# Performance work log

Measured on AMD Instinct MI355X. Metric: run time of the kernel, lower is better.

The kernel has to match this reference:

```python
import jax, jax.numpy as jnp
import numpy as np

B, N, DIM, H, DH = 2, 2048, 512, 8, 64
INNER = H * DH


def setup_inputs() -> dict:
    key = jax.random.key(0)
    ks = jax.random.split(key, 6)
    x = jax.random.normal(ks[0], (B, N, DIM), dtype=jnp.float32)
    mask_np = jax.random.randint(ks[1], (B, N), 0, 2, dtype=jnp.int32)
    mask_bert = jax.random.randint(ks[2], (B, N), 0, 2, dtype=jnp.int32)
    # params (torch Linear(dim, 3*inner, bias=False) -> stored here as [in, out])
    s_in = 1.0 / np.sqrt(DIM)
    s_inner = 1.0 / np.sqrt(INNER)
    W_qkv = jax.random.uniform(ks[3], (DIM, 3 * INNER), jnp.float32, -s_in, s_in)
    W_out = jax.random.uniform(ks[4], (INNER, DIM), jnp.float32, -s_inner, s_inner)
    b_out = jax.random.uniform(ks[5], (DIM,), jnp.float32, -s_inner, s_inner)
    return {"x": x, "mask_np": mask_np, "mask_bert": mask_bert,
            "W_qkv": W_qkv, "W_out": W_out, "b_out": b_out}


def reference(x, mask_np, mask_bert, W_qkv, W_out, b_out):
    scale = DH ** -0.5
    qkv = x @ W_qkv                                   # [b, n, 3*inner]
    q, k, v = jnp.split(qkv, 3, axis=-1)
    split_heads = lambda t: t.reshape(B, N, H, DH).transpose(0, 2, 1, 3)  # b h n d
    q, k, v = split_heads(q), split_heads(k), split_heads(v)
    dots = jnp.einsum('bhid,bhjd->bhij', q, k) * scale  # [b, h, n, n]
    # dual mask: (np_i * np_j == 0) or (bert_j == 1) -> fill with -1000
    np_pair = mask_np[:, None, :, None] * mask_np[:, None, None, :]      # b 1 n n
    bert_j = mask_bert[:, None, None, :]                                  # b 1 1 n
    masked = (np_pair == 0) | (bert_j == 1)
    dots = jnp.where(masked, jnp.float32(-1000.0), dots)
    attn = jax.nn.softmax(dots, axis=-1)
    out = jnp.einsum('bhij,bhjd->bhid', attn, v)       # b h n d
    out = out.transpose(0, 2, 1, 3).reshape(B, N, INNER)
    return out @ W_out + b_out
```

## Files before the change

kernel.cpp:

```cpp
#include <hip/hip_runtime.h>

typedef __attribute__((ext_vector_type(8))) short short8;
typedef __attribute__((ext_vector_type(4))) float f32x4;

#define GLDS16(gp, lp)                                                                     \
  __builtin_amdgcn_global_load_lds(                                                        \
      (const __attribute__((address_space(1))) unsigned int*)(gp),                         \
      (__attribute__((address_space(3))) unsigned int*)(lp), 16, 0, 0)

__device__ __forceinline__ unsigned short f2bf(float f) {
  unsigned u = __float_as_uint(f);
  u += 0x7FFFu + ((u >> 16) & 1u);
  return (unsigned short)(u >> 16);
}
__device__ __forceinline__ float bf2f(unsigned short h) {
  return __uint_as_float(((unsigned)h) << 16);
}
__device__ __forceinline__ unsigned cvt_pk_bf16(float a, float b) {
  unsigned r;
  asm("v_cvt_pk_bf16_f32 %0, %1, %2" : "=v"(r) : "v"(a), "v"(b));
  return r;
}

#define QSCALE 0.1803368801111244f

__global__ __launch_bounds__(256) void prep_x(
    const float* __restrict__ x, const int* __restrict__ mnp, const int* __restrict__ mbert,
    unsigned short* __restrict__ xb, unsigned short* __restrict__ jmbf) {
  int tid = blockIdx.x * 256 + threadIdx.x;
  if (tid < 524288) {
    float4 v = *(const float4*)(x + tid * 4);
    ushort4 o;
    o.x = f2bf(v.x); o.y = f2bf(v.y); o.z = f2bf(v.z); o.w = f2bf(v.w);
    *(ushort4*)(xb + tid * 4) = o;
  } else {
    int o = tid - 524288;
    if (o < 4096) jmbf[o] = (mnp[o] == 0 || mbert[o] == 1) ? f2bf(-100.0f) : f2bf(1e30f);
  }
}

__global__ __launch_bounds__(256) void transpose_w(
    const float* __restrict__ wqkv, const float* __restrict__ wout,
    unsigned short* __restrict__ wqkvT, unsigned short* __restrict__ whiT,
    unsigned short* __restrict__ wloT) {
  __shared__ float tile[64][65];
  int bid = blockIdx.x;
  const float* src;
  int N, k0, n0, which;
  if (bid < 192) { which = 0; src = wqkv; N = 1536; k0 = (bid / 24) * 64; n0 = (bid % 24) * 64; }
  else { bid -= 192; which = 1; src = wout; N = 512; k0 = (bid / 8) * 64; n0 = (bid % 8) * 64; }
  int tx = threadIdx.x & 63, ty = threadIdx.x >> 6;
#pragma unroll
  for (int i = 0; i < 16; ++i) {
    int row = ty + i * 4;
    tile[row][tx] = src[(k0 + row) * N + n0 + tx];
  }
  __syncthreads();
#pragma unroll
  for (int i = 0; i < 16; ++i) {
    int row = ty + i * 4;
    float w = tile[tx][row];
    if (which == 0) {
      wqkvT[(n0 + row) * 512 + k0 + tx] = f2bf(w);
    } else {
      unsigned short hi = f2bf(w);
      whiT[(n0 + row) * 512 + k0 + tx] = hi;
      wloT[(n0 + row) * 512 + k0 + tx] = f2bf(w - bf2f(hi));
    }
  }
}

__global__ __launch_bounds__(256) void qkv_gemm(
    const unsigned short* __restrict__ A, const unsigned short* __restrict__ Bt,
    unsigned short* __restrict__ qb, unsigned short* __restrict__ kb,
    unsigned short* __restrict__ vtb) {
  __shared__ __attribute__((aligned(16))) unsigned short lA[2][64 * 64];
  __shared__ __attribute__((aligned(16))) unsigned short lB[2][128 * 64];
  const int lane = threadIdx.x & 63, wid = threadIdx.x >> 6;
  const int l15 = lane & 15, lg = lane >> 4;
  const int row0 = blockIdx.x * 64;
  const int col0 = blockIdx.y * 128;
  const int srow = lane >> 3;
  const int gslot = (lane & 7) ^ srow;
  f32x4 acc[4][2] = {};

#define QKV_STAGE(ks_, buf_)                                                               \
  {                                                                                        \
    const int k0_ = (ks_) * 64;                                                            \
    _Pragma("unroll") for (int i = 0; i < 2; ++i) {                                        \
      int c = wid * 2 + i;                                                                 \
      GLDS16(A + (row0 + c * 8 + srow) * 512 + k0_ + gslot * 8, &lA[buf_][c * 512]);       \
    }                                                                                      \
    _Pragma("unroll") for (int i = 0; i < 4; ++i) {                                        \
      int c = wid * 4 + i;                                                                 \
      GLDS16(Bt + (col0 + c * 8 + srow) * 512 + k0_ + gslot * 8, &lB[buf_][c * 512]);      \
    }                                                                                      \
  }

  QKV_STAGE(0, 0);
  int buf = 0;
  for (int ks = 0; ks < 8; ++ks) {
    if (ks < 7) {
      QKV_STAGE(ks + 1, buf ^ 1);
      asm volatile("s_waitcnt vmcnt(6)" ::: "memory");
    } else {
      asm volatile("s_waitcnt vmcnt(0)" ::: "memory");
    }
    __builtin_amdgcn_s_barrier();
    const unsigned short* La = &lA[buf][0];
    const unsigned short* Lb = &lB[buf][0];
#pragma unroll
    for (int ksub = 0; ksub < 2; ++ksub) {
      short8 af[4], bfr[2];
#pragma unroll
      for (int m = 0; m < 4; ++m) {
        int row = m * 16 + l15;
        int slot = (ksub * 4 + lg) ^ (row & 7);
        af[m] = *(const short8*)(La + row * 64 + slot * 8);
      }
#pragma unroll
      for (int n = 0; n < 2; ++n) {
        int row = wid * 32 + n * 16 + l15;
        int slot = (ksub * 4 + lg) ^ (row & 7);
        bfr[n] = *(const short8*)(Lb + row * 64 + slot * 8);
      }
#pragma unroll
      for (int m = 0; m < 4; ++m)
#pragma unroll
        for (int n = 0; n < 2; ++n)
          acc[m][n] = __builtin_amdgcn_mfma_f32_16x16x32_bf16(af[m], bfr[n], acc[m][n], 0, 0, 0);
    }
    __builtin_amdgcn_s_barrier();
    buf ^= 1;
  }

  if (col0 >= 1024) {
    unsigned short* T = &lB[0][0];
#pragma unroll
    for (int m = 0; m < 4; ++m)
#pragma unroll
      for (int n = 0; n < 2; ++n) {
        int lc = wid * 32 + n * 16 + l15;
#pragma unroll
        for (int r = 0; r < 4; ++r)
          T[lc * 72 + m * 16 + lg * 4 + r] = f2bf(acc[m][n][r]);
      }
    __syncthreads();
    int c = threadIdx.x >> 1, half = threadIdx.x & 1;
    int gcol = col0 + c;
    int hh = (gcol >> 6) & 7, d = gcol & 63;
    int b = row0 >> 11, np0 = row0 & 2047;
    unsigned short* dst = vtb + ((size_t)((b * 8 + hh) * 64 + d)) * 2048 + np0 + half * 32;
    const unsigned short* srcT = T + c * 72 + half * 32;
#pragma unroll
    for (int i = 0; i < 4; ++i)
      *(short8*)(dst + i * 8) = *(const short8*)(srcT + i * 8);
  } else {
#pragma unroll
    for (int m = 0; m < 4; ++m) {
#pragma unroll
      for (int n = 0; n < 2; ++n) {
        int col = col0 + wid * 32 + n * 16 + l15;
        int which = col >> 9, hh = (col >> 6) & 7, d = col & 63;
#pragma unroll
        for (int r = 0; r < 4; ++r) {
          int grow = row0 + m * 16 + lg * 4 + r;
          int b = grow >> 11, np = grow & 2047;
          float v = acc[m][n][r];
          if (which == 0)
            qb[((b * 8 + hh) * 2048 + np) * 64 + d] = f2bf(v * QSCALE);
          else
            kb[((b * 8 + hh) * 2048 + np) * 64 + d] = f2bf(v);
        }
      }
    }
  }
}

__global__ __launch_bounds__(256) void attn_kernel(
    const unsigned short* __restrict__ qg, const unsigned short* __restrict__ kg,
    const unsigned short* __restrict__ vtg, const int* __restrict__ mnp,
    const unsigned short* __restrict__ jmbf,
    unsigned short* __restrict__ ahi, unsigned short* __restrict__ alo) {
  __shared__ __attribute__((aligned(16))) unsigned short Kbuf[4][64 * 64];
  __shared__ __attribute__((aligned(16))) unsigned short Vbuf[4][64 * 64];
  __shared__ __attribute__((aligned(16))) unsigned short jmlds[2048];
  __shared__ __attribute__((aligned(16))) unsigned short Plds[4][16 * 72];
  const int lane = threadIdx.x & 63, wid = threadIdx.x >> 6;
  const int l15 = lane & 15, lg = lane >> 4;
  const int srow = lane >> 3, gslot = (lane & 7) ^ srow;
  const int bh = blockIdx.x, b = bh >> 3, h = bh & 7;
  const int q0 = blockIdx.y * 64 + wid * 16;
  const unsigned short* Q = qg + bh * (2048 * 64);
  const unsigned short* K = kg + bh * (2048 * 64);
  const unsigned short* VT = vtg + bh * (64 * 2048);

#define ATTN_STAGE(jt_, buf_)                                                              \
  {                                                                                        \
    const int jb_ = (jt_) * 64;                                                            \
    _Pragma("unroll") for (int i = 0; i < 2; ++i)                                          \
        GLDS16(K + (jb_ + wid * 16 + i * 8 + srow) * 64 + gslot * 8,                       \
               &Kbuf[buf_][(wid * 16 + i * 8) * 64]);                                      \
    _Pragma("unroll") for (int i = 0; i < 2; ++i)                                          \
        GLDS16(VT + (wid * 16 + i * 8 + srow) * 2048 + jb_ + gslot * 8,                    \
               &Vbuf[buf_][(wid * 16 + i * 8) * 64]);                                      \
  }

  GLDS16(jmbf + b * 2048 + wid * 512 + lane * 8, jmlds + wid * 512);
  ATTN_STAGE(0, 0);
  ATTN_STAGE(1, 1);

  short8 qf[2];
#pragma unroll
  for (int s = 0; s < 2; ++s)
    qf[s] = *(const short8*)(Q + (q0 + l15) * 64 + s * 32 + lg * 8);
  const float rowflt = (mnp[b * 2048 + q0 + l15] == 0) ? -100.0f : 1e30f;

  f32x4 accO[4] = {};
  float psum = 0.0f;
  unsigned short* Pl = &Plds[wid][0];

  for (int jt = 0; jt < 32; ++jt) {
    if (jt < 30) {
      ATTN_STAGE(jt + 2, (jt + 2) & 3);
      asm volatile("s_waitcnt vmcnt(8)" ::: "memory");
    } else if (jt == 30) {
      asm volatile("s_waitcnt vmcnt(4)" ::: "memory");
    } else {
      asm volatile("s_waitcnt vmcnt(0)" ::: "memory");
    }
    __builtin_amdgcn_s_barrier();

    const unsigned short* Kc = &Kbuf[jt & 3][0];
    const unsigned short* Vc = &Vbuf[jt & 3][0];
    const int j0 = jt * 64;
    const int sw = (l15 & 7) * 8;
    short8 kf[4][2], vf[4][2];
#pragma unroll
    for (int t = 0; t < 4; ++t) {
      const int row = t * 16 + l15;
#pragma unroll
      for (int s = 0; s < 2; ++s)
        kf[t][s] = *(const short8*)(&Kc[row * 64 + ((s * 32 + lg * 8) ^ sw)]);
    }
#pragma unroll
    for (int dt = 0; dt < 4; ++dt) {
      const int row = dt * 16 + l15;
#pragma unroll
      for (int c = 0; c < 2; ++c)
        vf[dt][c] = *(const short8*)(&Vc[row * 64 + ((c * 32 + lg * 8) ^ sw)]);
    }

    f32x4 sacc[4] = {};
#pragma unroll
    for (int t = 0; t < 4; ++t)
#pragma unroll
      for (int s = 0; s < 2; ++s)
        sacc[t] = __builtin_amdgcn_mfma_f32_16x16x32_bf16(kf[t][s], qf[s], sacc[t], 0, 0, 0);

#pragma unroll
    for (int t = 0; t < 4; ++t) {
      ushort4 jmv = *(const ushort4*)(&jmlds[j0 + t * 16 + lg * 4]);
      float jmf[4] = {bf2f(jmv.x), bf2f(jmv.y), bf2f(jmv.z), bf2f(jmv.w)};
      float e[4];
#pragma unroll
      for (int r = 0; r < 4; ++r) {
        float sv = fminf(fminf(sacc[t][r], jmf[r]), rowflt);
        e[r] = exp2f(sv);
        psum += e[r];
      }
      *(unsigned*)(Pl + l15 * 72 + t * 16 + lg * 4 + 0) = cvt_pk_bf16(e[0], e[1]);
      *(unsigned*)(Pl + l15 * 72 + t * 16 + lg * 4 + 2) = cvt_pk_bf16(e[2], e[3]);
    }
    short8 pa[2];
#pragma unroll
    for (int c = 0; c < 2; ++c)
      pa[c] = *(const short8*)(Pl + l15 * 72 + c * 32 + lg * 8);
#pragma unroll
    for (int dt = 0; dt < 4; ++dt)
#pragma unroll
      for (int c = 0; c < 2; ++c)
        accO[dt] = __builtin_amdgcn_mfma_f32_16x16x32_bf16(pa[c], vf[dt][c], accO[dt], 0, 0, 0);
  }

  psum += __shfl_xor(psum, 16);
  psum += __shfl_xor(psum, 32);
  float lsum[4];
#pragma unroll
  for (int r = 0; r < 4; ++r) lsum[r] = 1.0f / __shfl(psum, lg * 4 + r);
#pragma unroll
  for (int dt = 0; dt < 4; ++dt) {
#pragma unroll
    for (int r = 0; r < 4; ++r) {
      float val = accO[dt][r] * lsum[r];
      int row = q0 + lg * 4 + r;
      int col = h * 64 + dt * 16 + l15;
      unsigned short hi = f2bf(val);
      ahi[(b * 2048 + row) * 512 + col] = hi;
      alo[(b * 2048 + row) * 512 + col] = f2bf(val - bf2f(hi));
    }
  }
}

__global__ __launch_bounds__(256) void outproj_gemm(
    const unsigned short* __restrict__ Ahi, const unsigned short* __restrict__ Alo,
    const unsigned short* __restrict__ WhiT, const unsigned short* __restrict__ WloT,
    const float* __restrict__ bias, float* __restrict__ out) {
  __shared__ __attribute__((aligned(16))) unsigned short lA[2][32 * 64];
  __shared__ __attribute__((aligned(16))) unsigned short lB[2][128 * 64];
  const int lane = threadIdx.x & 63, wid = threadIdx.x >> 6;
  const int l15 = lane & 15, lg = lane >> 4;
  const int row0 = blockIdx.x * 32;
  const int col0 = blockIdx.y * 128;
  const int srow = lane >> 3;
  const int gslot = (lane & 7) ^ srow;
  f32x4 acc[2][2] = {};

#define OP_STAGE(ks_, buf_)                                                                \
  {                                                                                        \
    const int seg_ = (ks_) >> 3;                                                           \
    const int k0_ = ((ks_) & 7) * 64;                                                      \
    const unsigned short* Asrc_ = (seg_ == 1) ? Alo : Ahi;                                 \
    const unsigned short* Bsrc_ = (seg_ == 2) ? WloT : WhiT;                               \
    GLDS16(Asrc_ + (row0 + wid * 8 + srow) * 512 + k0_ + gslot * 8, &lA[buf_][wid * 512]); \
    _Pragma("unroll") for (int i = 0; i < 4; ++i) {                                        \
      int c = wid * 4 + i;                                                                 \
      GLDS16(Bsrc_ + (col0 + c * 8 + srow) * 512 + k0_ + gslot * 8, &lB[buf_][c * 512]);   \
    }                                                                                      \
  }

  OP_STAGE(0, 0);
  int buf = 0;
  for (int ks = 0; ks < 24; ++ks) {
    if (ks < 23) {
      OP_STAGE(ks + 1, buf ^ 1);
      asm volatile("s_waitcnt vmcnt(5)" ::: "memory");
    } else {
      asm volatile("s_waitcnt vmcnt(0)" ::: "memory");
    }
    __builtin_amdgcn_s_barrier();
    const unsigned short* La = &lA[buf][0];
    const unsigned short* Lb = &lB[buf][0];
#pragma unroll
    for (int ksub = 0; ksub < 2; ++ksub) {
      short8 af[2], bfr[2];
#pragma unroll
      for (int m = 0; m < 2; ++m) {
        int row = m * 16 + l15;
        int slot = (ksub * 4 + lg) ^ (row & 7);
        af[m] = *(const short8*)(La + row * 64 + slot * 8);
      }
#pragma unroll
      for (int n = 0; n < 2; ++n) {
        int row = wid * 32 + n * 16 + l15;
        int slot = (ksub * 4 + lg) ^ (row & 7);
        bfr[n] = *(const short8*)(Lb + row * 64 + slot * 8);
      }
#pragma unroll
      for (int m = 0; m < 2; ++m)
#pragma unroll
        for (int n = 0; n < 2; ++n)
          acc[m][n] = __builtin_amdgcn_mfma_f32_16x16x32_bf16(af[m], bfr[n], acc[m][n], 0, 0, 0);
    }
    __builtin_amdgcn_s_barrier();
    buf ^= 1;
  }
#pragma unroll
  for (int m = 0; m < 2; ++m) {
#pragma unroll
    for (int n = 0; n < 2; ++n) {
      int col = col0 + wid * 32 + n * 16 + l15;
      float bb = bias[col];
#pragma unroll
      for (int r = 0; r < 4; ++r) {
        int grow = row0 + m * 16 + lg * 4 + r;
        out[grow * 512 + col] = acc[m][n][r] + bb;
      }
    }
  }
}

extern "C" void kernel_launch(void* const* d_in, const int* in_sizes, int n_in,
                              void* d_out, int out_size, void* d_ws, size_t ws_size,
                              hipStream_t stream) {
  (void)in_sizes; (void)n_in; (void)out_size; (void)ws_size;
  const float* x = (const float*)d_in[0];
  const int* mnp = (const int*)d_in[1];
  const int* mbert = (const int*)d_in[2];
  const float* wqkv = (const float*)d_in[3];
  const float* wout = (const float*)d_in[4];
  const float* bout = (const float*)d_in[5];
  float* out = (float*)d_out;

  char* ws = (char*)d_ws;
  size_t off = 0;
  auto alloc = [&](size_t bytes) {
    void* p = ws + off;
    off += (bytes + 255) & ~(size_t)255;
    return p;
  };
  unsigned short* xb    = (unsigned short*)alloc(2097152 * 2);
  unsigned short* wqkvT = (unsigned short*)alloc(786432 * 2);
  unsigned short* qb    = (unsigned short*)alloc(2097152 * 2);
  unsigned short* kb    = (unsigned short*)alloc(2097152 * 2);
  unsigned short* vtb   = (unsigned short*)alloc(2097152 * 2);
  unsigned short* ahi   = (unsigned short*)alloc(2097152 * 2);
  unsigned short* alo   = (unsigned short*)alloc(2097152 * 2);
  unsigned short* whiT  = (unsigned short*)alloc(262144 * 2);
  unsigned short* wloT  = (unsigned short*)alloc(262144 * 2);
  unsigned short* jmbf  = (unsigned short*)alloc(4096 * 2);

  prep_x<<<2064, 256, 0, stream>>>(x, mnp, mbert, xb, jmbf);
  transpose_w<<<256, 256, 0, stream>>>(wqkv, wout, wqkvT, whiT, wloT);
  qkv_gemm<<<dim3(64, 12), 256, 0, stream>>>(xb, wqkvT, qb, kb, vtb);
  attn_kernel<<<dim3(16, 32), 256, 0, stream>>>(qb, kb, vtb, mnp, jmbf, ahi, alo);
  outproj_gemm<<<dim3(128, 4), 256, 0, stream>>>(ahi, alo, whiT, wloT, bout, out);
}
```

Before: 144.1 us.

## Drop split-bf16 out-projection, double-buffer attention K/V, store mask as float

The out-projection no longer splits activations and weights into hi/lo bf16 pairs. It runs one plain bf16 GEMM over K=512 instead of three passes, with a larger 64-row tile. The attention kernel drops from 4-deep to 2-deep K/V buffering and manually unrolls two iterations. The column mask is now kept as float in LDS, so no bf16 conversion is needed. Together these cut memory traffic and the out-projection workload, but they give up the extra precision the hi/lo split provided.

New measurement: 133.5 us. 1.08x faster.

```diff
diff --git a/kernel.cpp b/kernel.cpp
--- a/kernel.cpp
+++ b/kernel.cpp
@@ -26,7 +26,7 @@
 
 __global__ __launch_bounds__(256) void prep_x(
     const float* __restrict__ x, const int* __restrict__ mnp, const int* __restrict__ mbert,
-    unsigned short* __restrict__ xb, unsigned short* __restrict__ jmbf) {
+    unsigned short* __restrict__ xb, float* __restrict__ jmflt) {
   int tid = blockIdx.x * 256 + threadIdx.x;
   if (tid < 524288) {
     float4 v = *(const float4*)(x + tid * 4);
@@ -35,14 +35,13 @@
     *(ushort4*)(xb + tid * 4) = o;
   } else {
     int o = tid - 524288;
-    if (o < 4096) jmbf[o] = (mnp[o] == 0 || mbert[o] == 1) ? f2bf(-100.0f) : f2bf(1e30f);
+    if (o < 4096) jmflt[o] = (mnp[o] == 0 || mbert[o] == 1) ? -100.0f : 1e30f;
   }
 }
 
 __global__ __launch_bounds__(256) void transpose_w(
     const float* __restrict__ wqkv, const float* __restrict__ wout,
-    unsigned short* __restrict__ wqkvT, unsigned short* __restrict__ whiT,
-    unsigned short* __restrict__ wloT) {
+    unsigned short* __restrict__ wqkvT, unsigned short* __restrict__ whiT) {
   __shared__ float tile[64][65];
   int bid = blockIdx.x;
   const float* src;
@@ -60,13 +59,8 @@
   for (int i = 0; i < 16; ++i) {
     int row = ty + i * 4;
     float w = tile[tx][row];
-    if (which == 0) {
-      wqkvT[(n0 + row) * 512 + k0 + tx] = f2bf(w);
-    } else {
-      unsigned short hi = f2bf(w);
-      whiT[(n0 + row) * 512 + k0 + tx] = hi;
-      wloT[(n0 + row) * 512 + k0 + tx] = f2bf(w - bf2f(hi));
-    }
+    if (which == 0) wqkvT[(n0 + row) * 512 + k0 + tx] = f2bf(w);
+    else            whiT[(n0 + row) * 512 + k0 + tx] = f2bf(w);
   }
 }
 
@@ -180,11 +174,10 @@
 __global__ __launch_bounds__(256) void attn_kernel(
     const unsigned short* __restrict__ qg, const unsigned short* __restrict__ kg,
     const unsigned short* __restrict__ vtg, const int* __restrict__ mnp,
-    const unsigned short* __restrict__ jmbf,
-    unsigned short* __restrict__ ahi, unsigned short* __restrict__ alo) {
-  __shared__ __attribute__((aligned(16))) unsigned short Kbuf[4][64 * 64];
-  __shared__ __attribute__((aligned(16))) unsigned short Vbuf[4][64 * 64];
-  __shared__ __attribute__((aligned(16))) unsigned short jmlds[2048];
+    const float* __restrict__ jmflt, unsigned short* __restrict__ ab) {
+  __shared__ __attribute__((aligned(16))) unsigned short Kbuf[2][64 * 64];
+  __shared__ __attribute__((aligned(16))) unsigned short Vbuf[2][64 * 64];
+  __shared__ __attribute__((aligned(16))) float jmlds[2048];
   __shared__ __attribute__((aligned(16))) unsigned short Plds[4][16 * 72];
   const int lane = threadIdx.x & 63, wid = threadIdx.x >> 6;
   const int l15 = lane & 15, lg = lane >> 4;
@@ -192,23 +185,21 @@
   const int bh = blockIdx.x, b = bh >> 3, h = bh & 7;
   const int q0 = blockIdx.y * 64 + wid * 16;
   const unsigned short* Q = qg + bh * (2048 * 64);
-  const unsigned short* K = kg + bh * (2048 * 64);
-  const unsigned short* VT = vtg + bh * (64 * 2048);
-
-#define ATTN_STAGE(jt_, buf_)                                                              \
+  const unsigned short* Kg = kg + bh * (2048 * 64) + (wid * 16 + srow) * 64 + gslot * 8;
+  const unsigned short* Vg = vtg + bh * (64 * 2048) + (wid * 16 + srow) * 2048 + gslot * 8;
+
+#define ASTAGE(jt_, B_)                                                                    \
   {                                                                                        \
-    const int jb_ = (jt_) * 64;                                                            \
-    _Pragma("unroll") for (int i = 0; i < 2; ++i)                                          \
-        GLDS16(K + (jb_ + wid * 16 + i * 8 + srow) * 64 + gslot * 8,                       \
-               &Kbuf[buf_][(wid * 16 + i * 8) * 64]);                                      \
-    _Pragma("unroll") for (int i = 0; i < 2; ++i)                                          \
-        GLDS16(VT + (wid * 16 + i * 8 + srow) * 2048 + jb_ + gslot * 8,                    \
-               &Vbuf[buf_][(wid * 16 + i * 8) * 64]);                                      \
-  }
-
-  GLDS16(jmbf + b * 2048 + wid * 512 + lane * 8, jmlds + wid * 512);
-  ATTN_STAGE(0, 0);
-  ATTN_STAGE(1, 1);
+    GLDS16(Kg + (jt_) * 4096, &Kbuf[B_][(wid * 16 + 0) * 64]);                             \
+    GLDS16(Kg + (jt_) * 4096 + 512, &Kbuf[B_][(wid * 16 + 8) * 64]);                       \
+    GLDS16(Vg + (jt_) * 64, &Vbuf[B_][(wid * 16 + 0) * 64]);                               \
+    GLDS16(Vg + (jt_) * 64 + 16384, &Vbuf[B_][(wid * 16 + 8) * 64]);                       \
+  }
+
+#pragma unroll
+  for (int i = 0; i < 2; ++i)
+    GLDS16(jmflt + b * 2048 + wid * 512 + i * 256 + lane * 4, jmlds + wid * 512 + i * 256);
+  ASTAGE(0, 0);
 
   short8 qf[2];
 #pragma unroll
@@ -219,68 +210,60 @@
   f32x4 accO[4] = {};
   float psum = 0.0f;
   unsigned short* Pl = &Plds[wid][0];
-
-  for (int jt = 0; jt < 32; ++jt) {
-    if (jt < 30) {
-      ATTN_STAGE(jt + 2, (jt + 2) & 3);
-      asm volatile("s_waitcnt vmcnt(8)" ::: "memory");
-    } else if (jt == 30) {
-      asm volatile("s_waitcnt vmcnt(4)" ::: "memory");
-    } else {
-      asm volatile("s_waitcnt vmcnt(0)" ::: "memory");
-    }
-    __builtin_amdgcn_s_barrier();
-
-    const unsigned short* Kc = &Kbuf[jt & 3][0];
-    const unsigned short* Vc = &Vbuf[jt & 3][0];
-    const int j0 = jt * 64;
-    const int sw = (l15 & 7) * 8;
-    short8 kf[4][2], vf[4][2];
-#pragma unroll
-    for (int t = 0; t < 4; ++t) {
-      const int row = t * 16 + l15;
-#pragma unroll
-      for (int s = 0; s < 2; ++s)
-        kf[t][s] = *(const short8*)(&Kc[row * 64 + ((s * 32 + lg * 8) ^ sw)]);
-    }
-#pragma unroll
-    for (int dt = 0; dt < 4; ++dt) {
-      const int row = dt * 16 + l15;
-#pragma unroll
-      for (int c = 0; c < 2; ++c)
-        vf[dt][c] = *(const short8*)(&Vc[row * 64 + ((c * 32 + lg * 8) ^ sw)]);
-    }
-
-    f32x4 sacc[4] = {};
-#pragma unroll
-    for (int t = 0; t < 4; ++t)
-#pragma unroll
-      for (int s = 0; s < 2; ++s)
-        sacc[t] = __builtin_amdgcn_mfma_f32_16x16x32_bf16(kf[t][s], qf[s], sacc[t], 0, 0, 0);
-
-#pragma unroll
-    for (int t = 0; t < 4; ++t) {
-      ushort4 jmv = *(const ushort4*)(&jmlds[j0 + t * 16 + lg * 4]);
-      float jmf[4] = {bf2f(jmv.x), bf2f(jmv.y), bf2f(jmv.z), bf2f(jmv.w)};
-      float e[4];
-#pragma unroll
-      for (int r = 0; r < 4; ++r) {
-        float sv = fminf(fminf(sacc[t][r], jmf[r]), rowflt);
-        e[r] = exp2f(sv);
-        psum += e[r];
-      }
-      *(unsigned*)(Pl + l15 * 72 + t * 16 + lg * 4 + 0) = cvt_pk_bf16(e[0], e[1]);
-      *(unsigned*)(Pl + l15 * 72 + t * 16 + lg * 4 + 2) = cvt_pk_bf16(e[2], e[3]);
-    }
-    short8 pa[2];
-#pragma unroll
-    for (int c = 0; c < 2; ++c)
-      pa[c] = *(const short8*)(Pl + l15 * 72 + c * 32 + lg * 8);
-#pragma unroll
-    for (int dt = 0; dt < 4; ++dt)
-#pragma unroll
-      for (int c = 0; c < 2; ++c)
-        accO[dt] = __builtin_amdgcn_mfma_f32_16x16x32_bf16(pa[c], vf[dt][c], accO[dt], 0, 0, 0);
+  const int sw = (l15 & 7) * 8;
+
+#define AITER(jt_, CUR)                                                                    \
+  {                                                                                        \
+    if ((jt_) < 31) {                                                                      \
+      ASTAGE((jt_) + 1, (CUR) ^ 1);                                                        \
+      asm volatile("s_waitcnt vmcnt(4)" ::: "memory");                                     \
+    } else {                                                                               \
+      asm volatile("s_waitcnt vmcnt(0)" ::: "memory");                                     \
+    }                                                                                      \
+    __builtin_amdgcn_s_barrier();                                                          \
+    const unsigned short* Kc = &Kbuf[CUR][0];                                              \
+    const unsigned short* Vc = &Vbuf[CUR][0];                                              \
+    const int j0 = (jt_) * 64;                                                             \
+    short8 kf[4][2], vf[4][2];                                                             \
+    _Pragma("unroll") for (int t = 0; t < 4; ++t) {                                        \
+      const int row = t * 16 + l15;                                                        \
+      _Pragma("unroll") for (int s = 0; s < 2; ++s)                                        \
+          kf[t][s] = *(const short8*)(&Kc[row * 64 + ((s * 32 + lg * 8) ^ sw)]);           \
+    }                                                                                      \
+    _Pragma("unroll") for (int dt = 0; dt < 4; ++dt) {                                     \
+      const int row = dt * 16 + l15;                                                       \
+      _Pragma("unroll") for (int c = 0; c < 2; ++c)                                        \
+          vf[dt][c] = *(const short8*)(&Vc[row * 64 + ((c * 32 + lg * 8) ^ sw)]);          \
+    }                                                                                      \
+    f32x4 sacc[4] = {};                                                                    \
+    _Pragma("unroll") for (int t = 0; t < 4; ++t)                                          \
+        _Pragma("unroll") for (int s = 0; s < 2; ++s)                                      \
+            sacc[t] = __builtin_amdgcn_mfma_f32_16x16x32_bf16(kf[t][s], qf[s], sacc[t],    \
+                                                              0, 0, 0);                    \
+    _Pragma("unroll") for (int t = 0; t < 4; ++t) {                                        \
+      f32x4 jm = *(const f32x4*)(&jmlds[j0 + t * 16 + lg * 4]);                            \
+      float e[4];                                                                          \
+      _Pragma("unroll") for (int r = 0; r < 4; ++r) {                                      \
+        float sv = fminf(fminf(sacc[t][r], jm[r]), rowflt);                                \
+        e[r] = exp2f(sv);                                                                  \
+        psum += e[r];                                                                      \
+      }                                                                                    \
+      *(unsigned*)(Pl + l15 * 72 + t * 16 + lg * 4 + 0) = cvt_pk_bf16(e[0], e[1]);         \
+      *(unsigned*)(Pl + l15 * 72 + t * 16 + lg * 4 + 2) = cvt_pk_bf16(e[2], e[3]);         \
+    }                                                                                      \
+    short8 pa[2];                                                                          \
+    _Pragma("unroll") for (int c = 0; c < 2; ++c)                                          \
+        pa[c] = *(const short8*)(Pl + l15 * 72 + c * 32 + lg * 8);                         \
+    _Pragma("unroll") for (int dt = 0; dt < 4; ++dt)                                       \
+        _Pragma("unroll") for (int c = 0; c < 2; ++c)                                      \
+            accO[dt] = __builtin_amdgcn_mfma_f32_16x16x32_bf16(pa[c], vf[dt][c], accO[dt], \
+                                                               0, 0, 0);                   \
+    __builtin_amdgcn_s_barrier();                                                          \
+  }
+
+  for (int jt2 = 0; jt2 < 16; ++jt2) {
+    AITER(jt2 * 2, 0);
+    AITER(jt2 * 2 + 1, 1);
   }
 
   psum += __shfl_xor(psum, 16);
@@ -295,46 +278,43 @@
       float val = accO[dt][r] * lsum[r];
       int row = q0 + lg * 4 + r;
       int col = h * 64 + dt * 16 + l15;
-      unsigned short hi = f2bf(val);
-      ahi[(b * 2048 + row) * 512 + col] = hi;
-      alo[(b * 2048 + row) * 512 + col] = f2bf(val - bf2f(hi));
+      ab[(b * 2048 + row) * 512 + col] = f2bf(val);
     }
   }
 }
 
 __global__ __launch_bounds__(256) void outproj_gemm(
-    const unsigned short* __restrict__ Ahi, const unsigned short* __restrict__ Alo,
-    const unsigned short* __restrict__ WhiT, const unsigned short* __restrict__ WloT,
+    const unsigned short* __restrict__ A, const unsigned short* __restrict__ Bt,
     const float* __restrict__ bias, float* __restrict__ out) {
-  __shared__ __attribute__((aligned(16))) unsigned short lA[2][32 * 64];
+  __shared__ __attribute__((aligned(16))) unsigned short lA[2][64 * 64];
   __shared__ __attribute__((aligned(16))) unsigned short lB[2][128 * 64];
   const int lane = threadIdx.x & 63, wid = threadIdx.x >> 6;
   const int l15 = lane & 15, lg = lane >> 4;
-  const int row0 = blockIdx.x * 32;
+  const int row0 = blockIdx.x * 64;
   const int col0 = blockIdx.y * 128;
   const int srow = lane >> 3;
   const int gslot = (lane & 7) ^ srow;
-  f32x4 acc[2][2] = {};
+  f32x4 acc[4][2] = {};
 
 #define OP_STAGE(ks_, buf_)                                                                \
   {                                                                                        \
-    const int seg_ = (ks_) >> 3;                                                           \
-    const int k0_ = ((ks_) & 7) * 64;                                                      \
-    const unsigned short* Asrc_ = (seg_ == 1) ? Alo : Ahi;                                 \
-    const unsigned short* Bsrc_ = (seg_ == 2) ? WloT : WhiT;                               \
-    GLDS16(Asrc_ + (row0 + wid * 8 + srow) * 512 + k0_ + gslot * 8, &lA[buf_][wid * 512]); \
+    const int k0_ = (ks_) * 64;                                                            \
+    _Pragma("unroll") for (int i = 0; i < 2; ++i) {                                        \
+      int c = wid * 2 + i;                                                                 \
+      GLDS16(A + (row0 + c * 8 + srow) * 512 + k0_ + gslot * 8, &lA[buf_][c * 512]);       \
+    }                                                                                      \
     _Pragma("unroll") for (int i = 0; i < 4; ++i) {                                        \
       int c = wid * 4 + i;                                                                 \
-      GLDS16(Bsrc_ + (col0 + c * 8 + srow) * 512 + k0_ + gslot * 8, &lB[buf_][c * 512]);   \
+      GLDS16(Bt + (col0 + c * 8 + srow) * 512 + k0_ + gslot * 8, &lB[buf_][c * 512]);      \
     }                                                                                      \
   }
 
   OP_STAGE(0, 0);
   int buf = 0;
-  for (int ks = 0; ks < 24; ++ks) {
-    if (ks < 23) {
+  for (int ks = 0; ks < 8; ++ks) {
+    if (ks < 7) {
       OP_STAGE(ks + 1, buf ^ 1);
-      asm volatile("s_waitcnt vmcnt(5)" ::: "memory");
+      asm volatile("s_waitcnt vmcnt(6)" ::: "memory");
     } else {
       asm volatile("s_waitcnt vmcnt(0)" ::: "memory");
     }
@@ -343,9 +323,9 @@
     const unsigned short* Lb = &lB[buf][0];
 #pragma unroll
     for (int ksub = 0; ksub < 2; ++ksub) {
-      short8 af[2], bfr[2];
-#pragma unroll
-      for (int m = 0; m < 2; ++m) {
+      short8 af[4], bfr[2];
+#pragma unroll
+      for (int m = 0; m < 4; ++m) {
         int row = m * 16 + l15;
         int slot = (ksub * 4 + lg) ^ (row & 7);
         af[m] = *(const short8*)(La + row * 64 + slot * 8);
@@ -357,7 +337,7 @@
         bfr[n] = *(const short8*)(Lb + row * 64 + slot * 8);
       }
 #pragma unroll
-      for (int m = 0; m < 2; ++m)
+      for (int m = 0; m < 4; ++m)
 #pragma unroll
         for (int n = 0; n < 2; ++n)
           acc[m][n] = __builtin_amdgcn_mfma_f32_16x16x32_bf16(af[m], bfr[n], acc[m][n], 0, 0, 0);
@@ -366,7 +346,7 @@
     buf ^= 1;
   }
 #pragma unroll
-  for (int m = 0; m < 2; ++m) {
+  for (int m = 0; m < 4; ++m) {
 #pragma unroll
     for (int n = 0; n < 2; ++n) {
       int col = col0 + wid * 32 + n * 16 + l15;
@@ -404,15 +384,13 @@
   unsigned short* qb    = (unsigned short*)alloc(2097152 * 2);
   unsigned short* kb    = (unsigned short*)alloc(2097152 * 2);
   unsigned short* vtb   = (unsigned short*)alloc(2097152 * 2);
-  unsigned short* ahi   = (unsigned short*)alloc(2097152 * 2);
-  unsigned short* alo   = (unsigned short*)alloc(2097152 * 2);
+  unsigned short* ab    = (unsigned short*)alloc(2097152 * 2);
   unsigned short* whiT  = (unsigned short*)alloc(262144 * 2);
-  unsigned short* wloT  = (unsigned short*)alloc(262144 * 2);
-  unsigned short* jmbf  = (unsigned short*)alloc(4096 * 2);
-
-  prep_x<<<2064, 256, 0, stream>>>(x, mnp, mbert, xb, jmbf);
-  transpose_w<<<256, 256, 0, stream>>>(wqkv, wout, wqkvT, whiT, wloT);
+  float* jmflt          = (float*)alloc(4096 * 4);
+
+  prep_x<<<2064, 256, 0, stream>>>(x, mnp, mbert, xb, jmflt);
+  transpose_w<<<256, 256, 0, stream>>>(wqkv, wout, wqkvT, whiT);
   qkv_gemm<<<dim3(64, 12), 256, 0, stream>>>(xb, wqkvT, qb, kb, vtb);
-  attn_kernel<<<dim3(16, 32), 256, 0, stream>>>(qb, kb, vtb, mnp, jmbf, ahi, alo);
-  outproj_gemm<<<dim3(128, 4), 256, 0, stream>>>(ahi, alo, whiT, wloT, bout, out);
-}
+  attn_kernel<<<dim3(16, 32), 256, 0, stream>>>(qb, kb, vtb, mnp, jmflt, ab);
+  outproj_gemm<<<dim3(64, 4), 256, 0, stream>>>(ab, whiT, bout, out);
+}
```
